# Kernel optimization log

Hardware: AMD Instinct MI355X
Metric: run time of the kernel (lower is better)

Reference implementation:

```python
import jax, jax.numpy as jnp
import numpy as np
import math

B, S, NV, D, VD = 2, 1024, 256, 4096, 768
H, KV, HD = 32, 4, 128
REP = H // KV
THETA, YSCALE, YALPHA, YBETA = 10000.0, 40.0, 1.0, 32.0
MAXSEQ = 2048
NEG = -1e30


def _yarn_cos_sin(n_pos):
    # YaRN-scaled RoPE tables, faithful to precompute_rope_yarn
    L_full = MAXSEQ * int(YSCALE)  # max_seq_len * yarn_scale as in __init__
    inv_freq = 1.0 / THETA ** (np.arange(0, HD, 2, dtype=np.float32) / HD)
    wavelengths = 2.0 * math.pi / inv_freq
    r = L_full / wavelengths
    gamma = np.clip((r - YALPHA) / (YBETA - YALPHA), 0.0, 1.0)
    inv_freq = inv_freq * ((1.0 - gamma) / YSCALE + gamma)
    freqs = np.outer(np.arange(n_pos, dtype=np.float32), inv_freq)
    emb = np.concatenate([freqs, freqs], axis=-1) / math.sqrt(0.1 * math.log(YSCALE) + 1.0)
    return jnp.asarray(np.cos(emb), jnp.float32), jnp.asarray(np.sin(emb), jnp.float32)


def setup_inputs() -> dict:
    key = jax.random.key(0)
    ks = jax.random.split(key, 7)
    x = jax.random.normal(ks[0], (B, S, D), jnp.float32)
    vision_features = jax.random.normal(ks[1], (B, NV, VD), jnp.float32)
    wq = jax.random.normal(ks[2], (H * HD, D), jnp.float32) * 0.02
    wk = jax.random.normal(ks[3], (KV * HD, D), jnp.float32) * 0.02
    wv = jax.random.normal(ks[4], (KV * HD, D), jnp.float32) * 0.02
    wo = jax.random.normal(ks[5], (D, H * HD), jnp.float32) * 0.02
    w_vision_kv = jax.random.normal(ks[6], (2 * KV * HD, VD), jnp.float32) * 0.02
    cos, sin = _yarn_cos_sin(S + NV)
    return {"x": x, "vision_features": vision_features, "wq": wq, "wk": wk,
            "wv": wv, "wo": wo, "w_vision_kv": w_vision_kv, "cos": cos, "sin": sin}


def _rotate_half(t):
    t1, t2 = t[..., : HD // 2], t[..., HD // 2 :]
    return jnp.concatenate([-t2, t1], axis=-1)


def reference(x, vision_features, wq, wk, wv, wo, w_vision_kv, cos, sin):
    b, s, _ = x.shape
    q = (x @ wq.T).reshape(b, s, H, HD)
    k = (x @ wk.T).reshape(b, s, KV, HD)
    v = (x @ wv.T).reshape(b, s, KV, HD)
    # vision KV prefix
    vkv = vision_features @ w_vision_kv.T  # [b, nv, 2*KV*HD]
    vk, vv = jnp.split(vkv, 2, axis=-1)
    nv = vision_features.shape[1]
    vk = vk.reshape(b, nv, KV, HD)
    vv = vv.reshape(b, nv, KV, HD)
    k = jnp.concatenate([vk, k], axis=1)  # [b, kvlen, KV, HD]
    v = jnp.concatenate([vv, v], axis=1)
    kvlen = k.shape[1]
    # RoPE (positions broadcast over heads)
    cq, sq = cos[None, :s, None, :], sin[None, :s, None, :]
    ck, sk = cos[None, :kvlen, None, :], sin[None, :kvlen, None, :]
    q = q * cq + _rotate_half(q) * sq
    k = k * ck + _rotate_half(k) * sk
    # GQA without materializing repeated K/V: group q heads by kv head
    qg = q.reshape(b, s, KV, REP, HD)
    scores = jnp.einsum("bsgrd,btgd->bgrst", qg, k) * (HD ** -0.5)
    # flash-style bottom-right causal: q pos i sees kv pos j <= i + (kvlen - s)
    i = jnp.arange(s)[:, None]
    j = jnp.arange(kvlen)[None, :]
    mask = j <= i + (kvlen - s)
    scores = jnp.where(mask, scores, NEG)
    probs = jax.nn.softmax(scores, axis=-1)
    out = jnp.einsum("bgrst,btgd->bsgrd", probs, v).reshape(b, s, H * HD)
    return out @ wo.T
```

## Files before the change

kernel.cpp:

```cpp
#include <hip/hip_runtime.h>
#include <hip/hip_bf16.h>
#include <cstdint>
#include <cstddef>

typedef short bf16x8 __attribute__((ext_vector_type(8)));
typedef float f32x4 __attribute__((ext_vector_type(4)));

__device__ __forceinline__ void gload_lds16(const void* g, void* l) {
  __builtin_amdgcn_global_load_lds((__attribute__((address_space(1))) const void*)g,
                                   (__attribute__((address_space(3))) void*)l, 16, 0, 0);
}

__device__ __forceinline__ unsigned short f2bf(float f) {
  unsigned u = __builtin_bit_cast(unsigned, f);
  u += 0x7fffu + ((u >> 16) & 1u);
  return (unsigned short)(u >> 16);
}
__device__ __forceinline__ float bf2f(unsigned short h) {
  unsigned u = ((unsigned)h) << 16;
  return __builtin_bit_cast(float, u);
}

struct CastPack {
  const float* s[7];
  unsigned short* d[7];
  int n4[7];
};
__global__ void k_cast_all(CastPack p) {
  const int tid0 = blockIdx.x * blockDim.x + threadIdx.x;
  const int stride = gridDim.x * blockDim.x;
#pragma unroll 1
  for (int seg = 0; seg < 7; ++seg) {
    const float4* __restrict__ src = reinterpret_cast<const float4*>(p.s[seg]);
    ushort4* __restrict__ dst = reinterpret_cast<ushort4*>(p.d[seg]);
    const int n4 = p.n4[seg];
    for (int i = tid0; i < n4; i += stride) {
      float4 v = src[i];
      ushort4 o;
      o.x = f2bf(v.x); o.y = f2bf(v.y); o.z = f2bf(v.z); o.w = f2bf(v.w);
      dst[i] = o;
    }
  }
}

__device__ __forceinline__ void storeC(float* C, size_t i, float v) { C[i] = v; }
__device__ __forceinline__ void storeC(unsigned short* C, size_t i, float v) { C[i] = f2bf(v); }

template <typename OutT>
__global__ __launch_bounds__(256) void k_gemm_bt(
    const unsigned short* __restrict__ A,
    const unsigned short* __restrict__ B,
    OutT* __restrict__ C,
    int M, int N, int K) {
  __shared__ __align__(16) unsigned short lA[128 * 64];
  __shared__ __align__(16) unsigned short lB[128 * 64];
  const int tid = threadIdx.x;
  const int w = tid >> 6, l = tid & 63;
  const int nwg = gridDim.x * gridDim.y;
  const int orig = blockIdx.y * gridDim.x + blockIdx.x;
  const int cpx = nwg >> 3;
  const int tile = (orig & 7) * cpx + (orig >> 3);
  const int m0 = (tile % gridDim.x) * 128;
  const int n0 = (tile / gridDim.x) * 128;
  const int wm = (w >> 1) * 64, wn = (w & 1) * 64;

  f32x4 acc[4][4];
#pragma unroll
  for (int i = 0; i < 4; ++i)
#pragma unroll
    for (int j = 0; j < 4; ++j) acc[i][j] = f32x4{0.f, 0.f, 0.f, 0.f};

  char* lAc = (char*)lA;
  char* lBc = (char*)lB;

  for (int k0 = 0; k0 < K; k0 += 64) {
#pragma unroll
    for (int p = 0; p < 4; ++p) {
      int r = (w * 4 + p) * 8 + (l >> 3);
      int c = (l & 7) ^ (r & 7);
      gload_lds16(A + (size_t)(m0 + r) * K + k0 + c * 8, lAc + (w * 4 + p) * 1024);
      gload_lds16(B + (size_t)(n0 + r) * K + k0 + c * 8, lBc + (w * 4 + p) * 1024);
    }
    __syncthreads();
#pragma unroll
    for (int kk = 0; kk < 2; ++kk) {
      bf16x8 af[4], bfr[4];
#pragma unroll
      for (int i = 0; i < 4; ++i) {
        int r = wm + i * 16 + (l & 15);
        int slot = (kk * 4 + (l >> 4)) ^ (r & 7);
        af[i] = *(const bf16x8*)(lAc + r * 128 + slot * 16);
      }
#pragma unroll
      for (int j = 0; j < 4; ++j) {
        int r = wn + j * 16 + (l & 15);
        int slot = (kk * 4 + (l >> 4)) ^ (r & 7);
        bfr[j] = *(const bf16x8*)(lBc + r * 128 + slot * 16);
      }
#pragma unroll
      for (int i = 0; i < 4; ++i)
#pragma unroll
        for (int j = 0; j < 4; ++j)
          acc[i][j] = __builtin_amdgcn_mfma_f32_16x16x32_bf16(af[i], bfr[j], acc[i][j], 0, 0, 0);
    }
    __syncthreads();
  }

#pragma unroll
  for (int i = 0; i < 4; ++i)
#pragma unroll
    for (int j = 0; j < 4; ++j) {
      int row = m0 + wm + i * 16 + (l >> 4) * 4;
      int col = n0 + wn + j * 16 + (l & 15);
#pragma unroll
      for (int r = 0; r < 4; ++r)
        storeC(C, (size_t)(row + r) * N + col, acc[i][j][r]);
    }
}

template <typename OutT>
__global__ __launch_bounds__(512) void k_gemm256x128(
    const unsigned short* __restrict__ A,
    const unsigned short* __restrict__ B,
    OutT* __restrict__ C,
    int M, int N, int K) {
  __shared__ __align__(16) unsigned short lA[2][2][256][32];
  __shared__ __align__(16) unsigned short lB[2][2][128][32];
  const int tid = threadIdx.x;
  const int w = tid >> 6, l = tid & 63;
  const int wr = w >> 2, wc = w & 3;
  const int lq = l & 15, g = l >> 4;
  const int fslot = (g ^ ((lq >> 1) & 3)) << 3;

  const int gm = M >> 8, gn = N >> 7;
  const int L = (int)blockIdx.x;
  const int xcd = L & 7, slot = L >> 3;
  const int m0 = (slot % gm) * 256;
  const int n0 = (xcd * (gn >> 3) + slot / gm) * 128;

  const unsigned short* Ap = A + (size_t)m0 * K;
  const unsigned short* Bp = B + (size_t)n0 * K;

  f32x4 acc[8][2];
#pragma unroll
  for (int i = 0; i < 8; ++i)
#pragma unroll
    for (int j = 0; j < 2; ++j) acc[i][j] = f32x4{0.f, 0.f, 0.f, 0.f};

  auto stageA = [&](unsigned short* lbase, int kcol) {
#pragma unroll
    for (int p = 0; p < 2; ++p) {
      int R = w * 32 + p * 16;
      int row = R + (l >> 2);
      int cc = ((l & 3) ^ ((l >> 3) & 3)) << 3;
      gload_lds16(Ap + (size_t)row * K + kcol + cc, lbase + R * 32);
    }
  };
  auto stageB = [&](unsigned short* lbase, int kcol) {
    int R = w * 16;
    int row = R + (l >> 2);
    int cc = ((l & 3) ^ ((l >> 3) & 3)) << 3;
    gload_lds16(Bp + (size_t)row * K + kcol + cc, lbase + R * 32);
  };

  const int nt = K >> 6;

  stageB(&lB[0][0][0][0], 0);
  stageA(&lA[0][0][0][0], 0);
  stageB(&lB[0][1][0][0], 32);
  stageA(&lA[0][1][0][0], 32);
  stageB(&lB[1][0][0][0], 64);
  stageA(&lA[1][0][0][0], 64);
  asm volatile("s_waitcnt vmcnt(3)" ::: "memory");
  __builtin_amdgcn_s_barrier();

  bf16x8 bfr[2], a[8];

  for (int T = 0; T < nt; ++T) {
    const int bf = T & 1, nb = bf ^ 1;

#pragma unroll
    for (int nf = 0; nf < 2; ++nf)
      bfr[nf] = *(const bf16x8*)&lB[bf][0][wc * 32 + nf * 16 + lq][fslot];
#pragma unroll
    for (int mf = 0; mf < 8; ++mf)
      a[mf] = *(const bf16x8*)&lA[bf][0][wr * 128 + mf * 16 + lq][fslot];
    if (T + 1 < nt) {
      stageA(&lA[nb][1][0][0], ((T + 1) << 6) + 32);
      stageB(&lB[nb][1][0][0], ((T + 1) << 6) + 32);
    }
    __builtin_amdgcn_s_barrier();
    asm volatile("s_waitcnt lgkmcnt(0)" ::: "memory");
    __builtin_amdgcn_s_setprio(1);
#pragma unroll
    for (int mf = 0; mf < 8; ++mf)
#pragma unroll
      for (int nf = 0; nf < 2; ++nf)
        acc[mf][nf] = __builtin_amdgcn_mfma_f32_16x16x32_bf16(a[mf], bfr[nf], acc[mf][nf], 0, 0, 0);
    __builtin_amdgcn_s_setprio(0);
    __builtin_amdgcn_s_barrier();

#pragma unroll
    for (int nf = 0; nf < 2; ++nf)
      bfr[nf] = *(const bf16x8*)&lB[bf][1][wc * 32 + nf * 16 + lq][fslot];
#pragma unroll
    for (int mf = 0; mf < 8; ++mf)
      a[mf] = *(const bf16x8*)&lA[bf][1][wr * 128 + mf * 16 + lq][fslot];
    if (T + 2 < nt) {
      stageA(&lA[bf][0][0][0], (T + 2) << 6);
      stageB(&lB[bf][0][0][0], (T + 2) << 6);
    }
    __builtin_amdgcn_s_barrier();
    asm volatile("s_waitcnt lgkmcnt(0)" ::: "memory");
    __builtin_amdgcn_s_setprio(1);
#pragma unroll
    for (int mf = 0; mf < 8; ++mf)
#pragma unroll
      for (int nf = 0; nf < 2; ++nf)
        acc[mf][nf] = __builtin_amdgcn_mfma_f32_16x16x32_bf16(a[mf], bfr[nf], acc[mf][nf], 0, 0, 0);
    __builtin_amdgcn_s_setprio(0);
    if (T < nt - 2)
      asm volatile("s_waitcnt vmcnt(3)" ::: "memory");
    else if (T == nt - 2)
      asm volatile("s_waitcnt vmcnt(0)" ::: "memory");
    __builtin_amdgcn_s_barrier();
  }

#pragma unroll
  for (int mf = 0; mf < 8; ++mf)
#pragma unroll
    for (int nf = 0; nf < 2; ++nf) {
      int row = m0 + wr * 128 + mf * 16 + g * 4;
      int col = n0 + wc * 32 + nf * 16 + lq;
#pragma unroll
      for (int r = 0; r < 4; ++r)
        storeC(C, (size_t)(row + r) * N + col, acc[mf][nf][r]);
    }
}

__global__ void k_post(unsigned short* __restrict__ qkv,
                       const unsigned short* __restrict__ vkv,
                       const float* __restrict__ cosT, const float* __restrict__ sinT,
                       unsigned short* __restrict__ k_all,
                       unsigned short* __restrict__ v_t) {
  int idx = blockIdx.x * blockDim.x + threadIdx.x;
  if (idx < 4194304) {
    int d0 = idx & 63;
    int h = (idx >> 6) & 31;
    int m = idx >> 11;
    int s = m & 1023;
    unsigned short* row = qkv + (size_t)m * 5120 + h * 128;
    float a = bf2f(row[d0]), b = bf2f(row[d0 + 64]);
    float c0 = cosT[s * 128 + d0], s0 = sinT[s * 128 + d0];
    float c1 = cosT[s * 128 + d0 + 64], s1 = sinT[s * 128 + d0 + 64];
    const float sc = 0.08838834764831845f;
    row[d0] = f2bf((a * c0 - b * s0) * sc);
    row[d0 + 64] = f2bf((b * c1 + a * s1) * sc);
  } else if (idx < 4194304 + 655360) {
    int i = idx - 4194304;
    int d0 = i & 63;
    int t = (i >> 6) % 1280;
    int bg = i / (64 * 1280);
    int b = bg >> 2, g = bg & 3;
    float a, bb;
    if (t < 256) {
      const unsigned short* src = vkv + (size_t)(b * 256 + t) * 1024 + g * 128;
      a = bf2f(src[d0]); bb = bf2f(src[d0 + 64]);
    } else {
      const unsigned short* src = qkv + (size_t)(b * 1024 + t - 256) * 5120 + 4096 + g * 128;
      a = bf2f(src[d0]); bb = bf2f(src[d0 + 64]);
    }
    float c0 = cosT[t * 128 + d0], s0 = sinT[t * 128 + d0];
    float c1 = cosT[t * 128 + d0 + 64], s1 = sinT[t * 128 + d0 + 64];
    unsigned short* dst = k_all + ((size_t)bg * 1280 + t) * 128;
    dst[d0] = f2bf(a * c0 - bb * s0);
    dst[d0 + 64] = f2bf(bb * c1 + a * s1);
  } else {
    int i = idx - 4194304 - 655360;
    int t = i % 1280;
    int d = (i / 1280) & 127;
    int bg = i / (1280 * 128);
    int b = bg >> 2, g = bg & 3;
    unsigned short v;
    if (t < 256) v = vkv[(size_t)(b * 256 + t) * 1024 + 512 + g * 128 + d];
    else         v = qkv[(size_t)(b * 1024 + t - 256) * 5120 + 4608 + g * 128 + d];
    v_t[(size_t)bg * 128 * 1280 + (size_t)d * 1280 + t] = v;
  }
}

__global__ __launch_bounds__(256) void k_attn(
    const unsigned short* __restrict__ qr,
    const unsigned short* __restrict__ k_all,
    const unsigned short* __restrict__ v_t,
    unsigned short* __restrict__ attn) {
  __shared__ __align__(16) unsigned short lK[2][64 * 128];
  __shared__ __align__(16) unsigned short lV[2][128 * 64];
  __shared__ __align__(16) unsigned short lPT[4][16][64];

  const int tid = threadIdx.x, w = tid >> 6, l = tid & 63;
  const int lq = l & 15, g = l >> 4;
  const int qb = (15 - (int)blockIdx.x) * 64;
  const int h = blockIdx.y, b = blockIdx.z;
  const int bg = b * 4 + (h >> 3);
  const unsigned short* kg = k_all + (size_t)bg * 1280 * 128;
  const unsigned short* vg = v_t + (size_t)bg * 128 * 1280;

  char* lKc = (char*)lK;
  char* lVc = (char*)lV;
  char* pbuf = (char*)&lPT[w][0][0];

  bf16x8 aq[4];
  {
    int row = qb + w * 16 + lq;
    const unsigned short* p = qr + (size_t)(b * 1024 + row) * 5120 + h * 128 + g * 8;
    aq[0] = *(const bf16x8*)(p);
    aq[1] = *(const bf16x8*)(p + 32);
    aq[2] = *(const bf16x8*)(p + 64);
    aq[3] = *(const bf16x8*)(p + 96);
  }

  f32x4 o[8];
#pragma unroll
  for (int i = 0; i < 8; ++i) o[i] = f32x4{0.f, 0.f, 0.f, 0.f};
  float mr = -1e30f;
  float lrp = 0.f;

  const int qrow_l = qb + w * 16 + lq;
  int tlim = qb + 320;
  if (tlim > 1280) tlim = 1280;
  const int nIter = tlim >> 6;

  auto stage = [&](int t0, int bufsel) {
#pragma unroll
    for (int p = 0; p < 4; ++p) {
      int r = (w * 4 + p) * 4 + (l >> 4);
      int c = (l & 15) ^ (r & 7);
      gload_lds16(kg + (size_t)(t0 + r) * 128 + c * 8,
                  lKc + bufsel * 16384 + (w * 4 + p) * 1024);
    }
#pragma unroll
    for (int p = 0; p < 4; ++p) {
      int d = (w * 4 + p) * 8 + (l >> 3);
      int c = (l & 7) ^ (d & 7);
      gload_lds16(vg + (size_t)d * 1280 + t0 + c * 8,
                  lVc + bufsel * 16384 + (w * 4 + p) * 1024);
    }
  };

  stage(0, 0);
  __syncthreads();

  int buf = 0;
  for (int it = 0; it < nIter; ++it) {
    const int t0 = it << 6;
    if (it + 1 < nIter) stage(t0 + 64, buf ^ 1);

    const char* kbase = lKc + buf * 16384;
    const char* vbase = lVc + buf * 16384;

    f32x4 sT[4];
#pragma unroll
    for (int sub = 0; sub < 4; ++sub) {
      f32x4 s4 = {0.f, 0.f, 0.f, 0.f};
      int krow = sub * 16 + lq;
      const char* kb = kbase + krow * 256;
#pragma unroll
      for (int kk = 0; kk < 4; ++kk) {
        int slot = (kk * 4 + g) ^ (krow & 7);
        bf16x8 kf = *(const bf16x8*)(kb + slot * 16);
        s4 = __builtin_amdgcn_mfma_f32_16x16x32_bf16(kf, aq[kk], s4, 0, 0, 0);
      }
      sT[sub] = s4;
    }

    if (t0 + 63 > qb + w * 16 + 256) {
#pragma unroll
      for (int sub = 0; sub < 4; ++sub)
#pragma unroll
        for (int r = 0; r < 4; ++r) {
          int t = t0 + sub * 16 + 4 * g + r;
          if (t > qrow_l + 256) sT[sub][r] = -1e30f;
        }
    }

    float pm = fmaxf(fmaxf(fmaxf(sT[0][0], sT[0][1]), fmaxf(sT[0][2], sT[0][3])),
                     fmaxf(fmaxf(sT[1][0], sT[1][1]), fmaxf(sT[1][2], sT[1][3])));
    pm = fmaxf(pm, fmaxf(fmaxf(fmaxf(sT[2][0], sT[2][1]), fmaxf(sT[2][2], sT[2][3])),
                         fmaxf(fmaxf(sT[3][0], sT[3][1]), fmaxf(sT[3][2], sT[3][3]))));
    pm = fmaxf(pm, __shfl_xor(pm, 16));
    pm = fmaxf(pm, __shfl_xor(pm, 32));

    if (!__all(pm <= mr + 8.0f)) {
      float mnew = fmaxf(mr, pm);
      float scl = __expf(mr - mnew);
      mr = mnew;
      lrp *= scl;
      float s0 = __shfl(scl, 4 * g + 0);
      float s1 = __shfl(scl, 4 * g + 1);
      float s2 = __shfl(scl, 4 * g + 2);
      float s3 = __shfl(scl, 4 * g + 3);
#pragma unroll
      for (int cs = 0; cs < 8; ++cs) {
        o[cs][0] *= s0; o[cs][1] *= s1; o[cs][2] *= s2; o[cs][3] *= s3;
      }
    }

#pragma unroll
    for (int sub = 0; sub < 4; ++sub) {
      float p0 = __expf(sT[sub][0] - mr);
      float p1 = __expf(sT[sub][1] - mr);
      float p2 = __expf(sT[sub][2] - mr);
      float p3 = __expf(sT[sub][3] - mr);
      lrp += (p0 + p1) + (p2 + p3);
      unsigned pk0, pk1;
      asm("v_cvt_pk_bf16_f32 %0, %1, %2" : "=v"(pk0) : "v"(p0), "v"(p1));
      asm("v_cvt_pk_bf16_f32 %0, %1, %2" : "=v"(pk1) : "v"(p2), "v"(p3));
      int c = (2 * sub + (g >> 1)) ^ (lq & 7);
      *(uint2*)(pbuf + lq * 128 + c * 16 + (g & 1) * 8) = make_uint2(pk0, pk1);
    }

    asm volatile("s_waitcnt lgkmcnt(0)" ::: "memory");
    __builtin_amdgcn_sched_barrier(0);

    bf16x8 pa0 = *(const bf16x8*)(pbuf + lq * 128 + ((g ^ (lq & 7)) * 16));
    bf16x8 pa1 = *(const bf16x8*)(pbuf + lq * 128 + (((4 + g) ^ (lq & 7)) * 16));

#pragma unroll
    for (int cs = 0; cs < 8; ++cs) {
      int drow = cs * 16 + lq;
      const char* vb = vbase + drow * 128;
      int s0i = g ^ (drow & 7);
      int s1i = (4 + g) ^ (drow & 7);
      bf16x8 v0 = *(const bf16x8*)(vb + s0i * 16);
      bf16x8 v1 = *(const bf16x8*)(vb + s1i * 16);
      o[cs] = __builtin_amdgcn_mfma_f32_16x16x32_bf16(pa0, v0, o[cs], 0, 0, 0);
      o[cs] = __builtin_amdgcn_mfma_f32_16x16x32_bf16(pa1, v1, o[cs], 0, 0, 0);
    }

    __syncthreads();
    buf ^= 1;
  }

  lrp += __shfl_xor(lrp, 16);
  lrp += __shfl_xor(lrp, 32);
  float inv = 1.0f / lrp;
  float invr[4];
  invr[0] = __shfl(inv, 4 * g + 0);
  invr[1] = __shfl(inv, 4 * g + 1);
  invr[2] = __shfl(inv, 4 * g + 2);
  invr[3] = __shfl(inv, 4 * g + 3);
#pragma unroll
  for (int cs = 0; cs < 8; ++cs)
#pragma unroll
    for (int r = 0; r < 4; ++r) {
      int row = qb + w * 16 + 4 * g + r;
      attn[(size_t)(b * 1024 + row) * 4096 + h * 128 + cs * 16 + lq] =
          f2bf(o[cs][r] * invr[r]);
    }
}

extern "C" void kernel_launch(void* const* d_in, const int* in_sizes, int n_in,
                              void* d_out, int out_size, void* d_ws, size_t ws_size,
                              hipStream_t stream) {
  const float* x    = (const float*)d_in[0];
  const float* vis  = (const float*)d_in[1];
  const float* wq   = (const float*)d_in[2];
  const float* wk   = (const float*)d_in[3];
  const float* wv   = (const float*)d_in[4];
  const float* wo   = (const float*)d_in[5];
  const float* wvkv = (const float*)d_in[6];
  const float* cosT = (const float*)d_in[7];
  const float* sinT = (const float*)d_in[8];
  float* out = (float*)d_out;
  char* ws = (char*)d_ws;

  size_t off = 0;
  auto alloc = [&](size_t b) { size_t r = off; off += (b + 255) & ~(size_t)255; return r; };
  unsigned short* wqkvb = (unsigned short*)(ws + alloc((size_t)5120 * 4096 * 2));
  unsigned short* wob   = (unsigned short*)(ws + alloc((size_t)4096 * 4096 * 2));
  unsigned short* wvkvb = (unsigned short*)(ws + alloc((size_t)1024 * 768 * 2));
  unsigned short* visb  = (unsigned short*)(ws + alloc((size_t)512 * 768 * 2));
  unsigned short* xb    = (unsigned short*)(ws + alloc((size_t)2048 * 4096 * 2));
  unsigned short* qkv   = (unsigned short*)(ws + alloc((size_t)2048 * 5120 * 2));
  unsigned short* vkvb  = (unsigned short*)(ws + alloc((size_t)512 * 1024 * 2));
  unsigned short* kall  = (unsigned short*)(ws + alloc((size_t)8 * 1280 * 128 * 2));
  unsigned short* vt    = (unsigned short*)(ws + alloc((size_t)8 * 128 * 1280 * 2));
  unsigned short* attnb = xb;
  if (ws_size < off) return;

  CastPack cp;
  cp.s[0] = x;    cp.d[0] = xb;                           cp.n4[0] = 2048 * 4096 / 4;
  cp.s[1] = wq;   cp.d[1] = wqkvb;                        cp.n4[1] = 4096 * 4096 / 4;
  cp.s[2] = wk;   cp.d[2] = wqkvb + (size_t)4096 * 4096;  cp.n4[2] = 512 * 4096 / 4;
  cp.s[3] = wv;   cp.d[3] = wqkvb + (size_t)4608 * 4096;  cp.n4[3] = 512 * 4096 / 4;
  cp.s[4] = wo;   cp.d[4] = wob;                          cp.n4[4] = 4096 * 4096 / 4;
  cp.s[5] = wvkv; cp.d[5] = wvkvb;                        cp.n4[5] = 1024 * 768 / 4;
  cp.s[6] = vis;  cp.d[6] = visb;                         cp.n4[6] = 512 * 768 / 4;
  k_cast_all<<<dim3(2048), dim3(256), 0, stream>>>(cp);

  k_gemm_bt<unsigned short><<<dim3(16, 40), dim3(256), 0, stream>>>(xb, wqkvb, qkv, 2048, 5120, 4096);
  k_gemm_bt<unsigned short><<<dim3(4, 8), dim3(256), 0, stream>>>(visb, wvkvb, vkvb, 512, 1024, 768);

  k_post<<<dim3(24064), dim3(256), 0, stream>>>(qkv, vkvb, cosT, sinT, kall, vt);

  k_attn<<<dim3(16, 32, 2), dim3(256), 0, stream>>>(qkv, kall, vt, attnb);

  k_gemm256x128<float><<<dim3(256), dim3(512), 0, stream>>>(attnb, wob, out, 2048, 4096, 4096);
}
```

Measured before the change: 341.1 us.

## Merge QKV and vision-KV GEMMs into one launch; pair causal q-blocks in attention

Folds the two projection GEMMs into a single 672-workgroup launch that picks its problem from the tile index. This removes a serial small launch and lets the 32 vision tiles fill the tail of the main GEMM. The attention kernel now has each workgroup process two query blocks (qpair and 15-qpair) back to back, so causal work is balanced across a grid half the size. The P staging buffer row stride is also padded from 128 to 144 bytes to reduce LDS bank conflicts. The risks are fewer attention workgroups in flight and extra per-block branching in the GEMM.

```diff
diff --git a/kernel.cpp b/kernel.cpp
--- a/kernel.cpp
+++ b/kernel.cpp
@@ -46,22 +46,34 @@
 __device__ __forceinline__ void storeC(float* C, size_t i, float v) { C[i] = v; }
 __device__ __forceinline__ void storeC(unsigned short* C, size_t i, float v) { C[i] = f2bf(v); }
 
-template <typename OutT>
-__global__ __launch_bounds__(256) void k_gemm_bt(
-    const unsigned short* __restrict__ A,
-    const unsigned short* __restrict__ B,
-    OutT* __restrict__ C,
-    int M, int N, int K) {
+__global__ __launch_bounds__(256) void k_gemm_qv(
+    const unsigned short* __restrict__ xb,
+    const unsigned short* __restrict__ wqkvb,
+    unsigned short* __restrict__ qkv,
+    const unsigned short* __restrict__ visb,
+    const unsigned short* __restrict__ wvkvb,
+    unsigned short* __restrict__ vkvb) {
   __shared__ __align__(16) unsigned short lA[128 * 64];
   __shared__ __align__(16) unsigned short lB[128 * 64];
   const int tid = threadIdx.x;
   const int w = tid >> 6, l = tid & 63;
-  const int nwg = gridDim.x * gridDim.y;
-  const int orig = blockIdx.y * gridDim.x + blockIdx.x;
-  const int cpx = nwg >> 3;
-  const int tile = (orig & 7) * cpx + (orig >> 3);
-  const int m0 = (tile % gridDim.x) * 128;
-  const int n0 = (tile / gridDim.x) * 128;
+  const int orig = (int)blockIdx.x;
+  const int tile = (orig & 7) * 84 + (orig >> 3);
+
+  const unsigned short* A;
+  const unsigned short* B;
+  unsigned short* C;
+  int K, N, m0, n0;
+  if (tile < 640) {
+    A = xb; B = wqkvb; C = qkv; K = 4096; N = 5120;
+    m0 = (tile & 15) * 128;
+    n0 = (tile >> 4) * 128;
+  } else {
+    int v = tile - 640;
+    A = visb; B = wvkvb; C = vkvb; K = 768; N = 1024;
+    m0 = (v & 3) * 128;
+    n0 = (v >> 2) * 128;
+  }
   const int wm = (w >> 1) * 64, wn = (w & 1) * 64;
 
   f32x4 acc[4][4];
@@ -295,11 +307,11 @@
     unsigned short* __restrict__ attn) {
   __shared__ __align__(16) unsigned short lK[2][64 * 128];
   __shared__ __align__(16) unsigned short lV[2][128 * 64];
-  __shared__ __align__(16) unsigned short lPT[4][16][64];
+  __shared__ __align__(16) unsigned short lPT[4][16][72];
 
   const int tid = threadIdx.x, w = tid >> 6, l = tid & 63;
   const int lq = l & 15, g = l >> 4;
-  const int qb = (15 - (int)blockIdx.x) * 64;
+  const int qpair = blockIdx.x;
   const int h = blockIdx.y, b = blockIdx.z;
   const int bg = b * 4 + (h >> 3);
   const unsigned short* kg = k_all + (size_t)bg * 1280 * 128;
@@ -308,27 +320,6 @@
   char* lKc = (char*)lK;
   char* lVc = (char*)lV;
   char* pbuf = (char*)&lPT[w][0][0];
-
-  bf16x8 aq[4];
-  {
-    int row = qb + w * 16 + lq;
-    const unsigned short* p = qr + (size_t)(b * 1024 + row) * 5120 + h * 128 + g * 8;
-    aq[0] = *(const bf16x8*)(p);
-    aq[1] = *(const bf16x8*)(p + 32);
-    aq[2] = *(const bf16x8*)(p + 64);
-    aq[3] = *(const bf16x8*)(p + 96);
-  }
-
-  f32x4 o[8];
-#pragma unroll
-  for (int i = 0; i < 8; ++i) o[i] = f32x4{0.f, 0.f, 0.f, 0.f};
-  float mr = -1e30f;
-  float lrp = 0.f;
-
-  const int qrow_l = qb + w * 16 + lq;
-  int tlim = qb + 320;
-  if (tlim > 1280) tlim = 1280;
-  const int nIter = tlim >> 6;
 
   auto stage = [&](int t0, int bufsel) {
 #pragma unroll
@@ -347,116 +338,139 @@
     }
   };
 
-  stage(0, 0);
-  __syncthreads();
-
   int buf = 0;
-  for (int it = 0; it < nIter; ++it) {
-    const int t0 = it << 6;
-    if (it + 1 < nIter) stage(t0 + 64, buf ^ 1);
-
-    const char* kbase = lKc + buf * 16384;
-    const char* vbase = lVc + buf * 16384;
-
-    f32x4 sT[4];
-#pragma unroll
-    for (int sub = 0; sub < 4; ++sub) {
-      f32x4 s4 = {0.f, 0.f, 0.f, 0.f};
-      int krow = sub * 16 + lq;
-      const char* kb = kbase + krow * 256;
-#pragma unroll
-      for (int kk = 0; kk < 4; ++kk) {
-        int slot = (kk * 4 + g) ^ (krow & 7);
-        bf16x8 kf = *(const bf16x8*)(kb + slot * 16);
-        s4 = __builtin_amdgcn_mfma_f32_16x16x32_bf16(kf, aq[kk], s4, 0, 0, 0);
-      }
-      sT[sub] = s4;
-    }
-
-    if (t0 + 63 > qb + w * 16 + 256) {
-#pragma unroll
-      for (int sub = 0; sub < 4; ++sub)
-#pragma unroll
-        for (int r = 0; r < 4; ++r) {
-          int t = t0 + sub * 16 + 4 * g + r;
-          if (t > qrow_l + 256) sT[sub][r] = -1e30f;
+#pragma unroll 1
+  for (int half = 0; half < 2; ++half) {
+    const int qb = (half ? (15 - qpair) : qpair) * 64;
+    const int qrow_l = qb + w * 16 + lq;
+    const int nIter = (qb + 320) >> 6;
+
+    bf16x8 aq[4];
+    {
+      int row = qb + w * 16 + lq;
+      const unsigned short* p = qr + (size_t)(b * 1024 + row) * 5120 + h * 128 + g * 8;
+      aq[0] = *(const bf16x8*)(p);
+      aq[1] = *(const bf16x8*)(p + 32);
+      aq[2] = *(const bf16x8*)(p + 64);
+      aq[3] = *(const bf16x8*)(p + 96);
+    }
+
+    f32x4 o[8];
+#pragma unroll
+    for (int i = 0; i < 8; ++i) o[i] = f32x4{0.f, 0.f, 0.f, 0.f};
+    float mr = -1e30f;
+    float lrp = 0.f;
+
+    stage(0, buf);
+    __syncthreads();
+
+    for (int it = 0; it < nIter; ++it) {
+      const int t0 = it << 6;
+      if (it + 1 < nIter) stage(t0 + 64, buf ^ 1);
+
+      const char* kbase = lKc + buf * 16384;
+      const char* vbase = lVc + buf * 16384;
+
+      f32x4 sT[4];
+#pragma unroll
+      for (int sub = 0; sub < 4; ++sub) {
+        f32x4 s4 = {0.f, 0.f, 0.f, 0.f};
+        int krow = sub * 16 + lq;
+        const char* kb = kbase + krow * 256;
+#pragma unroll
+        for (int kk = 0; kk < 4; ++kk) {
+          int slot = (kk * 4 + g) ^ (krow & 7);
+          bf16x8 kf = *(const bf16x8*)(kb + slot * 16);
+          s4 = __builtin_amdgcn_mfma_f32_16x16x32_bf16(kf, aq[kk], s4, 0, 0, 0);
         }
-    }
-
-    float pm = fmaxf(fmaxf(fmaxf(sT[0][0], sT[0][1]), fmaxf(sT[0][2], sT[0][3])),
-                     fmaxf(fmaxf(sT[1][0], sT[1][1]), fmaxf(sT[1][2], sT[1][3])));
-    pm = fmaxf(pm, fmaxf(fmaxf(fmaxf(sT[2][0], sT[2][1]), fmaxf(sT[2][2], sT[2][3])),
-                         fmaxf(fmaxf(sT[3][0], sT[3][1]), fmaxf(sT[3][2], sT[3][3]))));
-    pm = fmaxf(pm, __shfl_xor(pm, 16));
-    pm = fmaxf(pm, __shfl_xor(pm, 32));
-
-    if (!__all(pm <= mr + 8.0f)) {
-      float mnew = fmaxf(mr, pm);
-      float scl = __expf(mr - mnew);
-      mr = mnew;
-      lrp *= scl;
-      float s0 = __shfl(scl, 4 * g + 0);
-      float s1 = __shfl(scl, 4 * g + 1);
-      float s2 = __shfl(scl, 4 * g + 2);
-      float s3 = __shfl(scl, 4 * g + 3);
+        sT[sub] = s4;
+      }
+
+      if (t0 + 63 > qb + w * 16 + 256) {
+#pragma unroll
+        for (int sub = 0; sub < 4; ++sub)
+#pragma unroll
+          for (int r = 0; r < 4; ++r) {
+            int t = t0 + sub * 16 + 4 * g + r;
+            if (t > qrow_l + 256) sT[sub][r] = -1e30f;
+          }
+      }
+
+      float pm = fmaxf(fmaxf(fmaxf(sT[0][0], sT[0][1]), fmaxf(sT[0][2], sT[0][3])),
+                       fmaxf(fmaxf(sT[1][0], sT[1][1]), fmaxf(sT[1][2], sT[1][3])));
+      pm = fmaxf(pm, fmaxf(fmaxf(fmaxf(sT[2][0], sT[2][1]), fmaxf(sT[2][2], sT[2][3])),
+                           fmaxf(fmaxf(sT[3][0], sT[3][1]), fmaxf(sT[3][2], sT[3][3]))));
+      pm = fmaxf(pm, __shfl_xor(pm, 16));
+      pm = fmaxf(pm, __shfl_xor(pm, 32));
+
+      if (!__all(pm <= mr + 8.0f)) {
+        float mnew = fmaxf(mr, pm);
+        float scl = __expf(mr - mnew);
+        mr = mnew;
+        lrp *= scl;
+        float s0 = __shfl(scl, 4 * g + 0);
+        float s1 = __shfl(scl, 4 * g + 1);
+        float s2 = __shfl(scl, 4 * g + 2);
+        float s3 = __shfl(scl, 4 * g + 3);
+#pragma unroll
+        for (int cs = 0; cs < 8; ++cs) {
+          o[cs][0] *= s0; o[cs][1] *= s1; o[cs][2] *= s2; o[cs][3] *= s3;
+        }
+      }
+
+#pragma unroll
+      for (int sub = 0; sub < 4; ++sub) {
+        float p0 = __expf(sT[sub][0] - mr);
+        float p1 = __expf(sT[sub][1] - mr);
+        float p2 = __expf(sT[sub][2] - mr);
+        float p3 = __expf(sT[sub][3] - mr);
+        lrp += (p0 + p1) + (p2 + p3);
+        unsigned pk0, pk1;
+        asm("v_cvt_pk_bf16_f32 %0, %1, %2" : "=v"(pk0) : "v"(p0), "v"(p1));
+        asm("v_cvt_pk_bf16_f32 %0, %1, %2" : "=v"(pk1) : "v"(p2), "v"(p3));
+        int c = (2 * sub + (g >> 1)) ^ (lq & 7);
+        *(uint2*)(pbuf + lq * 144 + c * 16 + (g & 1) * 8) = make_uint2(pk0, pk1);
+      }
+
+      asm volatile("s_waitcnt lgkmcnt(0)" ::: "memory");
+      __builtin_amdgcn_sched_barrier(0);
+
+      bf16x8 pa0 = *(const bf16x8*)(pbuf + lq * 144 + ((g ^ (lq & 7)) * 16));
+      bf16x8 pa1 = *(const bf16x8*)(pbuf + lq * 144 + (((4 + g) ^ (lq & 7)) * 16));
+
 #pragma unroll
       for (int cs = 0; cs < 8; ++cs) {
-        o[cs][0] *= s0; o[cs][1] *= s1; o[cs][2] *= s2; o[cs][3] *= s3;
-      }
-    }
-
-#pragma unroll
-    for (int sub = 0; sub < 4; ++sub) {
-      float p0 = __expf(sT[sub][0] - mr);
-      float p1 = __expf(sT[sub][1] - mr);
-      float p2 = __expf(sT[sub][2] - mr);
-      float p3 = __expf(sT[sub][3] - mr);
-      lrp += (p0 + p1) + (p2 + p3);
-      unsigned pk0, pk1;
-      asm("v_cvt_pk_bf16_f32 %0, %1, %2" : "=v"(pk0) : "v"(p0), "v"(p1));
-      asm("v_cvt_pk_bf16_f32 %0, %1, %2" : "=v"(pk1) : "v"(p2), "v"(p3));
-      int c = (2 * sub + (g >> 1)) ^ (lq & 7);
-      *(uint2*)(pbuf + lq * 128 + c * 16 + (g & 1) * 8) = make_uint2(pk0, pk1);
-    }
-
-    asm volatile("s_waitcnt lgkmcnt(0)" ::: "memory");
-    __builtin_amdgcn_sched_barrier(0);
-
-    bf16x8 pa0 = *(const bf16x8*)(pbuf + lq * 128 + ((g ^ (lq & 7)) * 16));
-    bf16x8 pa1 = *(const bf16x8*)(pbuf + lq * 128 + (((4 + g) ^ (lq & 7)) * 16));
-
-#pragma unroll
-    for (int cs = 0; cs < 8; ++cs) {
-      int drow = cs * 16 + lq;
-      const char* vb = vbase + drow * 128;
-      int s0i = g ^ (drow & 7);
-      int s1i = (4 + g) ^ (drow & 7);
-      bf16x8 v0 = *(const bf16x8*)(vb + s0i * 16);
-      bf16x8 v1 = *(const bf16x8*)(vb + s1i * 16);
-      o[cs] = __builtin_amdgcn_mfma_f32_16x16x32_bf16(pa0, v0, o[cs], 0, 0, 0);
-      o[cs] = __builtin_amdgcn_mfma_f32_16x16x32_bf16(pa1, v1, o[cs], 0, 0, 0);
-    }
-
-    __syncthreads();
-    buf ^= 1;
+        int drow = cs * 16 + lq;
+        const char* vb = vbase + drow * 128;
+        int s0i = g ^ (drow & 7);
+        int s1i = (4 + g) ^ (drow & 7);
+        bf16x8 v0 = *(const bf16x8*)(vb + s0i * 16);
+        bf16x8 v1 = *(const bf16x8*)(vb + s1i * 16);
+        o[cs] = __builtin_amdgcn_mfma_f32_16x16x32_bf16(pa0, v0, o[cs], 0, 0, 0);
+        o[cs] = __builtin_amdgcn_mfma_f32_16x16x32_bf16(pa1, v1, o[cs], 0, 0, 0);
+      }
+
+      __syncthreads();
+      buf ^= 1;
+    }
+
+    lrp += __shfl_xor(lrp, 16);
+    lrp += __shfl_xor(lrp, 32);
+    float inv = 1.0f / lrp;
+    float invr[4];
+    invr[0] = __shfl(inv, 4 * g + 0);
+    invr[1] = __shfl(inv, 4 * g + 1);
+    invr[2] = __shfl(inv, 4 * g + 2);
+    invr[3] = __shfl(inv, 4 * g + 3);
+#pragma unroll
+    for (int cs = 0; cs < 8; ++cs)
+#pragma unroll
+      for (int r = 0; r < 4; ++r) {
+        int row = qb + w * 16 + 4 * g + r;
+        attn[(size_t)(b * 1024 + row) * 4096 + h * 128 + cs * 16 + lq] =
+            f2bf(o[cs][r] * invr[r]);
+      }
   }
-
-  lrp += __shfl_xor(lrp, 16);
-  lrp += __shfl_xor(lrp, 32);
-  float inv = 1.0f / lrp;
-  float invr[4];
-  invr[0] = __shfl(inv, 4 * g + 0);
-  invr[1] = __shfl(inv, 4 * g + 1);
-  invr[2] = __shfl(inv, 4 * g + 2);
-  invr[3] = __shfl(inv, 4 * g + 3);
-#pragma unroll
-  for (int cs = 0; cs < 8; ++cs)
-#pragma unroll
-    for (int r = 0; r < 4; ++r) {
-      int row = qb + w * 16 + 4 * g + r;
-      attn[(size_t)(b * 1024 + row) * 4096 + h * 128 + cs * 16 + lq] =
-          f2bf(o[cs][r] * invr[r]);
-    }
 }
 
 extern "C" void kernel_launch(void* const* d_in, const int* in_sizes, int n_in,
@@ -498,12 +512,11 @@
   cp.s[6] = vis;  cp.d[6] = visb;                         cp.n4[6] = 512 * 768 / 4;
   k_cast_all<<<dim3(2048), dim3(256), 0, stream>>>(cp);
 
-  k_gemm_bt<unsigned short><<<dim3(16, 40), dim3(256), 0, stream>>>(xb, wqkvb, qkv, 2048, 5120, 4096);
-  k_gemm_bt<unsigned short><<<dim3(4, 8), dim3(256), 0, stream>>>(visb, wvkvb, vkvb, 512, 1024, 768);
+  k_gemm_qv<<<dim3(672), dim3(256), 0, stream>>>(xb, wqkvb, qkv, visb, wvkvb, vkvb);
 
   k_post<<<dim3(24064), dim3(256), 0, stream>>>(qkv, vkvb, cosT, sinT, kall, vt);
 
-  k_attn<<<dim3(16, 32, 2), dim3(256), 0, stream>>>(qkv, kall, vt, attnb);
+  k_attn<<<dim3(8, 32, 2), dim3(256), 0, stream>>>(qkv, kall, vt, attnb);
 
   k_gemm256x128<float><<<dim3(256), dim3(512), 0, stream>>>(attnb, wob, out, 2048, 4096, 4096);
 }
```

Result: faster. 311.4 us (-8.7%).
